# Kernel optimization log

Measured on AMD Instinct MI355X. Metric: run time of the kernel, lower is better.

The kernel has to match this reference:

```python
import jax, jax.numpy as jnp
import numpy as np

# dims
N, Lx, Ff = 2048, 168, 64          # batch, encoder seq len, encoder features
HID = 256                           # GRU hidden size
Ly, Ft, FOUT, BINS = 72, 22, 10, 8  # decoder steps, future feats, output size, rain classes
DEC_IN = Ft + FOUT                  # 32, GRUCell input = cat(y_t, p)
REG_H, CLS_H = 128, 128             # head hidden widths
BETA = 1.1                          # SmeLU beta


def smelu(x):
    # SmeLU: 0 for x<=-b, x for x>=b, (x+b)^2/(4b) in between
    return jnp.where(x >= BETA, x,
                     jnp.where(x <= -BETA, jnp.zeros_like(x),
                               (x + BETA) ** 2 / (4.0 * BETA)))


def gru_step(h, u, Wih, Whh, bih, bhh):
    # torch GRU/GRUCell gate math; Wih: (3H, in), Whh: (3H, H)
    gi = u @ Wih.T + bih
    gh = h @ Whh.T + bhh
    i_r, i_z, i_n = jnp.split(gi, 3, axis=-1)
    h_r, h_z, h_n = jnp.split(gh, 3, axis=-1)
    r = jax.nn.sigmoid(i_r + h_r)
    z = jax.nn.sigmoid(i_z + h_z)
    n = jnp.tanh(i_n + r * h_n)
    return (1.0 - z) * n + z * h


def setup_inputs() -> dict:
    key = jax.random.key(0)
    ks = jax.random.split(key, 24)
    s = 1.0 / np.sqrt(HID)

    def rn(k, shape, scale):
        return jax.random.normal(k, shape, dtype=jnp.float32) * scale

    return {
        'x_f': rn(ks[0], (N, Lx, Ff), 1.0),
        'x': rn(ks[1], (N, Lx, FOUT), 1.0),      # unused by forward (matches torch)
        'y_t': rn(ks[2], (N, Ly + 1, Ft), 1.0),
        'p': rn(ks[3], (N, Ly + 1, FOUT), 1.0),
        # encoder GRU (1 layer, unidirectional)
        'enc_Wih': rn(ks[4], (3 * HID, Ff), s), 'enc_Whh': rn(ks[5], (3 * HID, HID), s),
        'enc_bih': rn(ks[6], (3 * HID,), s), 'enc_bhh': rn(ks[7], (3 * HID,), s),
        # decoder GRUCell
        'dec_Wih': rn(ks[8], (3 * HID, DEC_IN), s), 'dec_Whh': rn(ks[9], (3 * HID, HID), s),
        'dec_bih': rn(ks[10], (3 * HID,), s), 'dec_bhh': rn(ks[11], (3 * HID,), s),
        # temphr head: HID -> REG_H -> (FOUT - BINS)
        'th_W0': rn(ks[12], (REG_H, HID), s), 'th_b0': rn(ks[13], (REG_H,), s),
        'th_W1': rn(ks[14], (FOUT - BINS, REG_H), 1.0 / np.sqrt(REG_H)), 'th_b1': rn(ks[15], (FOUT - BINS,), 0.05),
        # class head: HID -> CLS_H -> BINS
        'cl_W0': rn(ks[16], (CLS_H, HID), s), 'cl_b0': rn(ks[17], (CLS_H,), s),
        'cl_W1': rn(ks[18], (BINS, CLS_H), 1.0 / np.sqrt(CLS_H)), 'cl_b1': rn(ks[19], (BINS,), 0.05),
    }


def reference(x_f, x, y_t, p,
              enc_Wih, enc_Whh, enc_bih, enc_bhh,
              dec_Wih, dec_Whh, dec_bih, dec_bhh,
              th_W0, th_b0, th_W1, th_b1,
              cl_W0, cl_b0, cl_W1, cl_b1):
    # ---- encoder: run GRU over Lx, keep final hidden (N, HID) ----
    h0 = jnp.zeros((x_f.shape[0], HID), dtype=x_f.dtype)
    enc_xs = jnp.swapaxes(x_f, 0, 1)  # (Lx, N, Ff)

    def enc_body(h, u):
        return gru_step(h, u, enc_Wih, enc_Whh, enc_bih, enc_bhh), None

    h_enc, _ = jax.lax.scan(enc_body, h0, enc_xs)

    # ---- decoder inputs: torch loop uses cat(y_t,p) at index 0, then i-1 ----
    ytp = jnp.concatenate([y_t[:, :-1, :], p[:, :-1, :]], axis=-1)  # (N, Ly, DEC_IN)
    idx = jnp.concatenate([jnp.zeros((1,), jnp.int32), jnp.arange(Ly - 1, dtype=jnp.int32)])
    dec_in = jnp.swapaxes(ytp[:, idx, :], 0, 1)  # (Ly, N, DEC_IN)

    def dec_body(h, u):
        h2 = gru_step(h, u, dec_Wih, dec_Whh, dec_bih, dec_bhh)
        th = smelu(h2 @ th_W0.T + th_b0) @ th_W1.T + th_b1   # (N, 2)
        cl = smelu(h2 @ cl_W0.T + cl_b0) @ cl_W1.T + cl_b1   # (N, BINS)
        return h2, jnp.concatenate([th, cl], axis=-1)

    _, outs = jax.lax.scan(dec_body, h_enc, dec_in)  # (Ly, N, FOUT)
    return jnp.swapaxes(outs, 0, 1)  # (N, Ly, FOUT)
```

## Files before the change

kernel.cpp:

```cpp
#include <hip/hip_runtime.h>

typedef __bf16 v8bf __attribute__((ext_vector_type(8)));
typedef float v4f __attribute__((ext_vector_type(4)));
typedef float v4ff __attribute__((ext_vector_type(4)));
typedef unsigned short u16;
typedef unsigned int u32;

#define DEVI __device__ __forceinline__

constexpr int LX = 168, FF = 64;
constexpr int LY = 72, FT = 22, FOUTC = 10;
constexpr int HID = 256;
constexpr int HSTR = 264;
constexpr int UST2 = 40;
constexpr int SSTR = 264;

constexpr int W_EWIH = 0;
constexpr int W_EWHH = 49152;
constexpr int W_DWIH = 245760;
constexpr int W_DWHH = 270336;
constexpr int W_THW0 = 466944;
constexpr int W_THW1 = 499712;
constexpr int W_CLW0 = 499968;
constexpr int W_CLW1 = 532736;
constexpr int W_TOTAL = 533760;

DEVI u16 f2bf(float f) {
  u32 x; __builtin_memcpy(&x, &f, 4);
  return (u16)((x + 0x7FFFu + ((x >> 16) & 1u)) >> 16);
}
DEVI float sigm(float x) { return __builtin_amdgcn_rcpf(1.f + __expf(-x)); }
DEVI float tanh_(float x) {
  float e = __expf(-2.f * fabsf(x));
  return copysignf((1.f - e) * __builtin_amdgcn_rcpf(1.f + e), x);
}
DEVI float smelu_(float x) {
  if (x >= 1.1f) return x;
  if (x <= -1.1f) return 0.f;
  float u = x + 1.1f;
  return u * u * (1.f / 4.4f);
}
DEVI v8bf ld8(const u16* p) { return *reinterpret_cast<const v8bf*>(p); }
DEVI v4f ldw(const u16* p) { return *reinterpret_cast<const v4f*>(p); }
DEVI v8bf asbf(v4f x) { return __builtin_bit_cast(v8bf, x); }
DEVI void pin(v4f& x) { asm("" : "+v"(x)); }
DEVI v4f mfma16(v8bf a, v8bf b, v4f c) {
  return __builtin_amdgcn_mfma_f32_16x16x32_bf16(a, b, c, 0, 0, 0);
}
DEVI v8bf cvt2f(v4ff lo, v4ff hi) {
  v8bf r;
#pragma unroll
  for (int j = 0; j < 4; ++j) { r[j] = (__bf16)lo[j]; r[4 + j] = (__bf16)hi[j]; }
  return r;
}

__global__ void cvt_weights(const float* __restrict__ eWih, const float* __restrict__ eWhh,
                            const float* __restrict__ dWih, const float* __restrict__ dWhh,
                            const float* __restrict__ thW0, const float* __restrict__ thW1,
                            const float* __restrict__ clW0, const float* __restrict__ clW1,
                            u16* __restrict__ ws) {
  const int i = blockIdx.x * 256 + threadIdx.x;
  if (i >= W_TOTAL) return;
  const float* src; int off;
  if      (i < W_EWHH) { src = eWih; off = W_EWIH; }
  else if (i < W_DWIH) { src = eWhh; off = W_EWHH; }
  else if (i < W_DWHH) { src = dWih; off = W_DWIH; }
  else if (i < W_THW0) { src = dWhh; off = W_DWHH; }
  else if (i < W_THW1) { src = thW0; off = W_THW0; }
  else if (i < W_CLW0) { src = thW1; off = W_THW1; }
  else if (i < W_CLW1) { src = clW0; off = W_CLW0; }
  else                 { src = clW1; off = W_CLW1; }
  ws[i] = f2bf(src[i - off]);
}

__global__ __launch_bounds__(512, 2) void encdec_kernel(
    const float* __restrict__ xf, const float* __restrict__ yt, const float* __restrict__ pp,
    const float* __restrict__ ebih, const float* __restrict__ ebhh,
    const float* __restrict__ dbih, const float* __restrict__ dbhh,
    const float* __restrict__ thb0, const float* __restrict__ thb1,
    const float* __restrict__ clb0, const float* __restrict__ clb1,
    const u16* __restrict__ ws, float* __restrict__ outp) {
  __shared__ __align__(16) u16 slab[256 * SSTR];
  __shared__ __align__(16) u16 hls[2][16 * HSTR];
  __shared__ __align__(16) u16 a1x[16 * HSTR];
  __shared__ __align__(16) u16 uls[2][16 * UST2];

  const u16* eWih = ws + W_EWIH;
  const u16* eWhh = ws + W_EWHH;
  const u16* dWih = ws + W_DWIH;
  const u16* dWhh = ws + W_DWHH;
  const u16* thW0 = ws + W_THW0;
  const u16* thW1 = ws + W_THW1;
  const u16* clW0 = ws + W_CLW0;
  const u16* clW1 = ws + W_CLW1;

  const int tid = threadIdx.x;
  const int wave = tid >> 6;
  const int lane = tid & 63;
  const int col16 = lane & 15;
  const int quad = lane >> 4;
  const int n0 = blockIdx.x * 16;

  for (int i = tid; i < 16 * HSTR; i += 512) hls[0][i] = 0;

  float hreg[2][4];
#pragma unroll
  for (int j = 0; j < 2; ++j)
#pragma unroll
    for (int r = 0; r < 4; ++r) hreg[j][r] = 0.f;

  v4f wz[2][8], wn[2][8];
  float bsr[2], bsz[2], bin_[2], bhn[2];

  {
    for (int i = tid; i < 256 * 32; i += 512) {
      const int row = i >> 5, kb = (i & 31) << 3;
      *reinterpret_cast<v8bf*>(&slab[row * SSTR + kb]) = ld8(eWhh + row * HID + kb);
    }
#pragma unroll
    for (int j = 0; j < 2; ++j) {
      const int c = wave + 8 * j;
      const int mr = c * 16 + col16, mz = 256 + mr, mn = 512 + mr;
#pragma unroll
      for (int k = 0; k < 8; ++k) {
        wz[j][k] = ldw(eWhh + (size_t)mz * HID + k * 32 + quad * 8); pin(wz[j][k]);
        wn[j][k] = ldw(eWhh + (size_t)mn * HID + k * 32 + quad * 8); pin(wn[j][k]);
      }
      bsr[j] = ebih[mr] + ebhh[mr];
      bsz[j] = ebih[mz] + ebhh[mz];
      bin_[j] = ebih[mn];
      bhn[j] = ebhh[mn];
    }
    const float* xbase = xf + (size_t)(n0 + col16) * LX * FF + quad * 8;
    const u16* sp0 = slab + (wave * 16 + col16) * SSTR + quad * 8;
    const u16* sp1 = slab + ((wave + 8) * 16 + col16) * SSTR + quad * 8;

    v8bf xa0, xa1;
    {
      const v4ff x0 = *(const v4ff*)(xbase);
      const v4ff x1 = *(const v4ff*)(xbase + 4);
      const v4ff x2 = *(const v4ff*)(xbase + 32);
      const v4ff x3 = *(const v4ff*)(xbase + 36);
      xa0 = cvt2f(x0, x1);
      xa1 = cvt2f(x2, x3);
    }
    __syncthreads();

#pragma unroll 1
    for (int t = 0; t < LX; ++t) {
      const u16* hb = hls[t & 1] + col16 * HSTR + quad * 8;

      v4f az[2], ar[2], an[2], ai[2];
#pragma unroll
      for (int j = 0; j < 2; ++j) {
        az[j] = (v4f){bsz[j], bsz[j], bsz[j], bsz[j]};
        ar[j] = (v4f){bsr[j], bsr[j], bsr[j], bsr[j]};
        an[j] = (v4f){bhn[j], bhn[j], bhn[j], bhn[j]};
        ai[j] = (v4f){bin_[j], bin_[j], bin_[j], bin_[j]};
      }

      __builtin_amdgcn_s_setprio(1);
      v8bf ak = ld8(hb), ak1 = ld8(hb + 32);
#pragma unroll
      for (int k = 0; k < 8; ++k) {
        az[0] = mfma16(ak, asbf(wz[0][k]), az[0]);
        az[1] = mfma16(ak, asbf(wz[1][k]), az[1]);
        ar[0] = mfma16(ak, ld8(sp0 + k * 32), ar[0]);
        ar[1] = mfma16(ak, ld8(sp1 + k * 32), ar[1]);
        an[0] = mfma16(ak, asbf(wn[0][k]), an[0]);
        an[1] = mfma16(ak, asbf(wn[1][k]), an[1]);
        ak = ak1;
        if (k < 6) ak1 = ld8(hb + (k + 2) * 32);
      }

      const int tn = (t + 1 < LX) ? t + 1 : 0;
      const float* xr = xbase + (size_t)tn * FF;
      const v4ff x0 = *(const v4ff*)(xr);
      const v4ff x1 = *(const v4ff*)(xr + 4);
      const v4ff x2 = *(const v4ff*)(xr + 32);
      const v4ff x3 = *(const v4ff*)(xr + 36);

#pragma unroll
      for (int j = 0; j < 2; ++j) {
        const int m = (wave + 8 * j) * 16 + col16;
        const u16* pwr = eWih + (size_t)m * FF + quad * 8;
        const u16* pwz = eWih + (size_t)(256 + m) * FF + quad * 8;
        const u16* pwn = eWih + (size_t)(512 + m) * FF + quad * 8;
        az[j] = mfma16(xa0, ld8(pwz), az[j]);
        az[j] = mfma16(xa1, ld8(pwz + 32), az[j]);
        ar[j] = mfma16(xa0, ld8(pwr), ar[j]);
        ar[j] = mfma16(xa1, ld8(pwr + 32), ar[j]);
        ai[j] = mfma16(xa0, ld8(pwn), ai[j]);
        ai[j] = mfma16(xa1, ld8(pwn + 32), ai[j]);
      }
      __builtin_amdgcn_s_setprio(0);

#pragma unroll
      for (int j = 0; j < 2; ++j) {
        const int cidx = (wave + 8 * j) * 16 + col16;
#pragma unroll
        for (int r = 0; r < 4; ++r) {
          const float zg = sigm(az[j][r]);
          const float rg = sigm(ar[j][r]);
          const float ng = tanh_(ai[j][r] + rg * an[j][r]);
          hreg[j][r] = (1.f - zg) * ng + zg * hreg[j][r];
          hls[(t + 1) & 1][(quad * 4 + r) * HSTR + cidx] = f2bf(hreg[j][r]);
        }
      }
      xa0 = cvt2f(x0, x1);
      xa1 = cvt2f(x2, x3);
      __syncthreads();
    }
  }

  {
    for (int i = tid; i < 256 * 32; i += 512) {
      const int row = i >> 5, kb = (i & 31) << 3;
      *reinterpret_cast<v8bf*>(&slab[row * SSTR + kb]) = ld8(dWhh + row * HID + kb);
    }
    float hb0[2];
#pragma unroll
    for (int j = 0; j < 2; ++j) {
      const int c = wave + 8 * j;
      const int mr = c * 16 + col16, mz = 256 + mr, mn = 512 + mr;
#pragma unroll
      for (int k = 0; k < 8; ++k) {
        wz[j][k] = ldw(dWhh + (size_t)mz * HID + k * 32 + quad * 8); pin(wz[j][k]);
        wn[j][k] = ldw(dWhh + (size_t)mn * HID + k * 32 + quad * 8); pin(wn[j][k]);
      }
      bsr[j] = dbih[mr] + dbhh[mr];
      bsz[j] = dbih[mz] + dbhh[mz];
      bin_[j] = dbih[mn];
      bhn[j] = dbhh[mn];
      const int ml = wave * 16 + col16;
      hb0[j] = (j == 0) ? thb0[ml] : clb0[ml];
    }
    const bool w1th = (col16 < 2);
    const bool w1cl = (col16 >= 2 && col16 < FOUTC);
    const float b1v = w1th ? thb1[col16] : (w1cl ? clb1[col16 - 2] : 0.f);
    const u16* sp0 = slab + (wave * 16 + col16) * SSTR + quad * 8;
    const u16* sp1 = slab + ((wave + 8) * 16 + col16) * SSTR + quad * 8;

    const int srr = tid >> 5, scc = tid & 31;
    const size_t ybase = (size_t)(n0 + srr) * (LY + 1);
    {
      const float v = (scc < FT) ? yt[ybase * FT + scc] : pp[ybase * FOUTC + (scc - FT)];
      uls[0][srr * UST2 + scc] = f2bf(v);
    }
    __syncthreads();

#pragma unroll 1
    for (int t = 0; t < LY; ++t) {
      float un = 0.f;
      if (t + 1 < LY)
        un = (scc < FT) ? yt[(ybase + t) * FT + scc]
                        : pp[(ybase + t) * FOUTC + (scc - FT)];
      const v8bf ua = ld8(uls[t & 1] + col16 * UST2 + quad * 8);
      const u16* hb = hls[0] + col16 * HSTR + quad * 8;
      v8bf a[8];
#pragma unroll
      for (int k = 0; k < 8; ++k) a[k] = ld8(hb + k * 32);
      __syncthreads();

      if (wave == 0 && t >= 2) {
        const u16* arow = ((t & 1) ? a1x : hls[1]) + col16 * HSTR + quad * 8;
        v4f acc = {b1v, b1v, b1v, b1v};
#pragma unroll
        for (int kt = 0; kt < 8; ++kt) {
          v8bf b;
#pragma unroll
          for (int j = 0; j < 8; ++j) b[j] = (__bf16)0.0f;
          if (kt < 4) { if (w1th) b = ld8(thW1 + col16 * 128 + kt * 32 + quad * 8); }
          else        { if (w1cl) b = ld8(clW1 + (col16 - 2) * 128 + (kt - 4) * 32 + quad * 8); }
          acc = mfma16(ld8(arow + kt * 32), b, acc);
        }
        if (col16 < FOUTC) {
#pragma unroll
          for (int r = 0; r < 4; ++r)
            outp[((size_t)(n0 + quad * 4 + r) * LY + (t - 2)) * FOUTC + col16] = acc[r];
        }
      }

      v4f az[2], ar[2], an[2], ai[2];
#pragma unroll
      for (int j = 0; j < 2; ++j) {
        az[j] = (v4f){bsz[j], bsz[j], bsz[j], bsz[j]};
        ar[j] = (v4f){bsr[j], bsr[j], bsr[j], bsr[j]};
        an[j] = (v4f){bhn[j], bhn[j], bhn[j], bhn[j]};
        ai[j] = (v4f){bin_[j], bin_[j], bin_[j], bin_[j]};
      }
      __builtin_amdgcn_s_setprio(1);
#pragma unroll
      for (int k = 0; k < 8; ++k) {
        az[0] = mfma16(a[k], asbf(wz[0][k]), az[0]);
        az[1] = mfma16(a[k], asbf(wz[1][k]), az[1]);
        ar[0] = mfma16(a[k], ld8(sp0 + k * 32), ar[0]);
        ar[1] = mfma16(a[k], ld8(sp1 + k * 32), ar[1]);
        an[0] = mfma16(a[k], asbf(wn[0][k]), an[0]);
        an[1] = mfma16(a[k], asbf(wn[1][k]), an[1]);
      }
#pragma unroll
      for (int j = 0; j < 2; ++j) {
        const int m = (wave + 8 * j) * 16 + col16;
        az[j] = mfma16(ua, ld8(dWih + (size_t)(256 + m) * 32 + quad * 8), az[j]);
        ar[j] = mfma16(ua, ld8(dWih + (size_t)m * 32 + quad * 8), ar[j]);
        ai[j] = mfma16(ua, ld8(dWih + (size_t)(512 + m) * 32 + quad * 8), ai[j]);
      }
      __builtin_amdgcn_s_setprio(0);
#pragma unroll
      for (int j = 0; j < 2; ++j) {
        const int cidx = (wave + 8 * j) * 16 + col16;
#pragma unroll
        for (int r = 0; r < 4; ++r) {
          const float zg = sigm(az[j][r]);
          const float rg = sigm(ar[j][r]);
          const float ng = tanh_(ai[j][r] + rg * an[j][r]);
          hreg[j][r] = (1.f - zg) * ng + zg * hreg[j][r];
          hls[0][(quad * 4 + r) * HSTR + cidx] = f2bf(hreg[j][r]);
        }
      }

      if (t >= 1) {
        u16* a1w = ((t - 1) & 1) ? a1x : hls[1];
#pragma unroll
        for (int j = 0; j < 2; ++j) {
          const u16* W0 = (j == 0) ? thW0 : clW0;
          const u16* pw = W0 + (size_t)(wave * 16 + col16) * HID + quad * 8;
          v4f acc = {hb0[j], hb0[j], hb0[j], hb0[j]};
#pragma unroll
          for (int k = 0; k < 8; ++k) acc = mfma16(a[k], ld8(pw + k * 32), acc);
          const int c = wave + 8 * j;
#pragma unroll
          for (int r = 0; r < 4; ++r)
            a1w[(quad * 4 + r) * HSTR + c * 16 + col16] = f2bf(smelu_(acc[r]));
        }
      }
      if (t + 1 < LY) uls[(t + 1) & 1][srr * UST2 + scc] = f2bf(un);
      __syncthreads();
    }

    {
      const u16* h2b = hls[0] + col16 * HSTR + quad * 8;
      v8bf ah2[8];
#pragma unroll
      for (int k = 0; k < 8; ++k) ah2[k] = ld8(h2b + k * 32);
      u16* a1w = ((LY - 1) & 1) ? a1x : hls[1];
#pragma unroll
      for (int j = 0; j < 2; ++j) {
        const u16* W0 = (j == 0) ? thW0 : clW0;
        const u16* pw = W0 + (size_t)(wave * 16 + col16) * HID + quad * 8;
        v4f acc = {hb0[j], hb0[j], hb0[j], hb0[j]};
#pragma unroll
        for (int k = 0; k < 8; ++k) acc = mfma16(ah2[k], ld8(pw + k * 32), acc);
        const int c = wave + 8 * j;
#pragma unroll
        for (int r = 0; r < 4; ++r)
          a1w[(quad * 4 + r) * HSTR + c * 16 + col16] = f2bf(smelu_(acc[r]));
      }
      if (wave == 0) {
        const u16* arow = (((LY - 2) & 1) ? a1x : hls[1]) + col16 * HSTR + quad * 8;
        v4f acc = {b1v, b1v, b1v, b1v};
#pragma unroll
        for (int kt = 0; kt < 8; ++kt) {
          v8bf b;
#pragma unroll
          for (int j = 0; j < 8; ++j) b[j] = (__bf16)0.0f;
          if (kt < 4) { if (w1th) b = ld8(thW1 + col16 * 128 + kt * 32 + quad * 8); }
          else        { if (w1cl) b = ld8(clW1 + (col16 - 2) * 128 + (kt - 4) * 32 + quad * 8); }
          acc = mfma16(ld8(arow + kt * 32), b, acc);
        }
        if (col16 < FOUTC) {
#pragma unroll
          for (int r = 0; r < 4; ++r)
            outp[((size_t)(n0 + quad * 4 + r) * LY + (LY - 2)) * FOUTC + col16] = acc[r];
        }
      }
      __syncthreads();
      if (wave == 0) {
        const u16* arow = (((LY - 1) & 1) ? a1x : hls[1]) + col16 * HSTR + quad * 8;
        v4f acc = {b1v, b1v, b1v, b1v};
#pragma unroll
        for (int kt = 0; kt < 8; ++kt) {
          v8bf b;
#pragma unroll
          for (int j = 0; j < 8; ++j) b[j] = (__bf16)0.0f;
          if (kt < 4) { if (w1th) b = ld8(thW1 + col16 * 128 + kt * 32 + quad * 8); }
          else        { if (w1cl) b = ld8(clW1 + (col16 - 2) * 128 + (kt - 4) * 32 + quad * 8); }
          acc = mfma16(ld8(arow + kt * 32), b, acc);
        }
        if (col16 < FOUTC) {
#pragma unroll
          for (int r = 0; r < 4; ++r)
            outp[((size_t)(n0 + quad * 4 + r) * LY + (LY - 1)) * FOUTC + col16] = acc[r];
        }
      }
    }
  }
}

extern "C" void kernel_launch(void* const* d_in, const int* in_sizes, int n_in,
                              void* d_out, int out_size, void* d_ws, size_t ws_size,
                              hipStream_t stream) {
  (void)in_sizes; (void)n_in; (void)ws_size; (void)out_size;
  const float* xf   = (const float*)d_in[0];
  const float* yt   = (const float*)d_in[2];
  const float* pp   = (const float*)d_in[3];
  const float* eWih = (const float*)d_in[4];
  const float* eWhh = (const float*)d_in[5];
  const float* ebih = (const float*)d_in[6];
  const float* ebhh = (const float*)d_in[7];
  const float* dWih = (const float*)d_in[8];
  const float* dWhh = (const float*)d_in[9];
  const float* dbih = (const float*)d_in[10];
  const float* dbhh = (const float*)d_in[11];
  const float* thW0 = (const float*)d_in[12];
  const float* thb0 = (const float*)d_in[13];
  const float* thW1 = (const float*)d_in[14];
  const float* thb1 = (const float*)d_in[15];
  const float* clW0 = (const float*)d_in[16];
  const float* clb0 = (const float*)d_in[17];
  const float* clW1 = (const float*)d_in[18];
  const float* clb1 = (const float*)d_in[19];
  float* outp = (float*)d_out;
  u16* ws = (u16*)d_ws;

  cvt_weights<<<dim3((W_TOTAL + 255) / 256), dim3(256), 0, stream>>>(
      eWih, eWhh, dWih, dWhh, thW0, thW1, clW0, clW1, ws);
  encdec_kernel<<<dim3(128), dim3(512), 0, stream>>>(
      xf, yt, pp, ebih, ebhh, dbih, dbhh, thb0, thb1, clb0, clb1, ws, outp);
}
```

Before: 1.344 ms.

## Halve workgroup to 4 waves, keep more Whh rows in registers

After: 1.970 ms. 1.47x slower.

```diff
diff --git a/kernel.cpp b/kernel.cpp
--- a/kernel.cpp
+++ b/kernel.cpp
@@ -73,16 +73,16 @@
   ws[i] = f2bf(src[i - off]);
 }
 
-__global__ __launch_bounds__(512, 2) void encdec_kernel(
+__global__ __launch_bounds__(256, 1) void encdec_kernel(
     const float* __restrict__ xf, const float* __restrict__ yt, const float* __restrict__ pp,
     const float* __restrict__ ebih, const float* __restrict__ ebhh,
     const float* __restrict__ dbih, const float* __restrict__ dbhh,
     const float* __restrict__ thb0, const float* __restrict__ thb1,
     const float* __restrict__ clb0, const float* __restrict__ clb1,
     const u16* __restrict__ ws, float* __restrict__ outp) {
-  __shared__ __align__(16) u16 slab[256 * SSTR];
+  __shared__ __align__(16) u16 slab[128 * SSTR];
   __shared__ __align__(16) u16 hls[2][16 * HSTR];
-  __shared__ __align__(16) u16 a1x[16 * HSTR];
+  __shared__ __align__(16) u16 a1d[2][16 * HSTR];
   __shared__ __align__(16) u16 uls[2][16 * UST2];
 
   const u16* eWih = ws + W_EWIH;
@@ -101,25 +101,30 @@
   const int quad = lane >> 4;
   const int n0 = blockIdx.x * 16;
 
-  for (int i = tid; i < 16 * HSTR; i += 512) hls[0][i] = 0;
-
-  float hreg[2][4];
-#pragma unroll
-  for (int j = 0; j < 2; ++j)
+  float hreg[4][4];
+#pragma unroll
+  for (int j = 0; j < 4; ++j)
 #pragma unroll
     for (int r = 0; r < 4; ++r) hreg[j][r] = 0.f;
 
-  v4f wz[2][8], wn[2][8];
-  float bsr[2], bsz[2], bin_[2], bhn[2];
+  v4f wz[4][8], wn[4][8], wr[2][8];
+  float bsr[4], bsz[4], bin_[4], bhn[4];
+
+  const u16* sp2 = slab + ((wave * 2 + 0) * 16 + col16) * SSTR + quad * 8;
+  const u16* sp3 = slab + ((wave * 2 + 1) * 16 + col16) * SSTR + quad * 8;
 
   {
-    for (int i = tid; i < 256 * 32; i += 512) {
-      const int row = i >> 5, kb = (i & 31) << 3;
-      *reinterpret_cast<v8bf*>(&slab[row * SSTR + kb]) = ld8(eWhh + row * HID + kb);
-    }
-#pragma unroll
-    for (int j = 0; j < 2; ++j) {
-      const int c = wave + 8 * j;
+    for (int i = tid; i < 128 * 32; i += 256) {
+      const int sr = i >> 5, kb = (i & 31) << 3;
+      const int ct = sr >> 4;
+      const int c = (ct >> 1) * 4 + 2 + (ct & 1);
+      const int m = c * 16 + (sr & 15);
+      *reinterpret_cast<v8bf*>(&slab[sr * SSTR + kb]) = ld8(eWhh + (size_t)m * HID + kb);
+    }
+    for (int i = tid; i < 16 * HSTR; i += 256) hls[0][i] = 0;
+#pragma unroll
+    for (int j = 0; j < 4; ++j) {
+      const int c = wave * 4 + j;
       const int mr = c * 16 + col16, mz = 256 + mr, mn = 512 + mr;
 #pragma unroll
       for (int k = 0; k < 8; ++k) {
@@ -131,9 +136,15 @@
       bin_[j] = ebih[mn];
       bhn[j] = ebhh[mn];
     }
+#pragma unroll
+    for (int j = 0; j < 2; ++j) {
+      const int mr = (wave * 4 + j) * 16 + col16;
+#pragma unroll
+      for (int k = 0; k < 8; ++k) {
+        wr[j][k] = ldw(eWhh + (size_t)mr * HID + k * 32 + quad * 8); pin(wr[j][k]);
+      }
+    }
     const float* xbase = xf + (size_t)(n0 + col16) * LX * FF + quad * 8;
-    const u16* sp0 = slab + (wave * 16 + col16) * SSTR + quad * 8;
-    const u16* sp1 = slab + ((wave + 8) * 16 + col16) * SSTR + quad * 8;
 
     v8bf xa0, xa1;
     {
@@ -149,43 +160,40 @@
 #pragma unroll 1
     for (int t = 0; t < LX; ++t) {
       const u16* hb = hls[t & 1] + col16 * HSTR + quad * 8;
-
-      v4f az[2], ar[2], an[2], ai[2];
-#pragma unroll
-      for (int j = 0; j < 2; ++j) {
+      v8bf a[8];
+#pragma unroll
+      for (int k = 0; k < 8; ++k) a[k] = ld8(hb + k * 32);
+
+      v4f az[4], ar[4], an[4];
+#pragma unroll
+      for (int j = 0; j < 4; ++j) {
         az[j] = (v4f){bsz[j], bsz[j], bsz[j], bsz[j]};
         ar[j] = (v4f){bsr[j], bsr[j], bsr[j], bsr[j]};
         an[j] = (v4f){bhn[j], bhn[j], bhn[j], bhn[j]};
-        ai[j] = (v4f){bin_[j], bin_[j], bin_[j], bin_[j]};
-      }
-
-      __builtin_amdgcn_s_setprio(1);
-      v8bf ak = ld8(hb), ak1 = ld8(hb + 32);
-#pragma unroll
-      for (int k = 0; k < 8; ++k) {
-        az[0] = mfma16(ak, asbf(wz[0][k]), az[0]);
-        az[1] = mfma16(ak, asbf(wz[1][k]), az[1]);
-        ar[0] = mfma16(ak, ld8(sp0 + k * 32), ar[0]);
-        ar[1] = mfma16(ak, ld8(sp1 + k * 32), ar[1]);
-        an[0] = mfma16(ak, asbf(wn[0][k]), an[0]);
-        an[1] = mfma16(ak, asbf(wn[1][k]), an[1]);
-        ak = ak1;
-        if (k < 6) ak1 = ld8(hb + (k + 2) * 32);
-      }
-
-      const int tn = (t + 1 < LX) ? t + 1 : 0;
-      const float* xr = xbase + (size_t)tn * FF;
-      const v4ff x0 = *(const v4ff*)(xr);
-      const v4ff x1 = *(const v4ff*)(xr + 4);
-      const v4ff x2 = *(const v4ff*)(xr + 32);
-      const v4ff x3 = *(const v4ff*)(xr + 36);
-
-#pragma unroll
-      for (int j = 0; j < 2; ++j) {
-        const int m = (wave + 8 * j) * 16 + col16;
+      }
+#pragma unroll
+      for (int k = 0; k < 8; ++k) {
+        az[0] = mfma16(a[k], asbf(wz[0][k]), az[0]);
+        az[1] = mfma16(a[k], asbf(wz[1][k]), az[1]);
+        az[2] = mfma16(a[k], asbf(wz[2][k]), az[2]);
+        az[3] = mfma16(a[k], asbf(wz[3][k]), az[3]);
+        ar[0] = mfma16(a[k], asbf(wr[0][k]), ar[0]);
+        ar[1] = mfma16(a[k], asbf(wr[1][k]), ar[1]);
+        ar[2] = mfma16(a[k], ld8(sp2 + k * 32), ar[2]);
+        ar[3] = mfma16(a[k], ld8(sp3 + k * 32), ar[3]);
+        an[0] = mfma16(a[k], asbf(wn[0][k]), an[0]);
+        an[1] = mfma16(a[k], asbf(wn[1][k]), an[1]);
+        an[2] = mfma16(a[k], asbf(wn[2][k]), an[2]);
+        an[3] = mfma16(a[k], asbf(wn[3][k]), an[3]);
+      }
+      v4f ai[4];
+#pragma unroll
+      for (int j = 0; j < 4; ++j) {
+        const int m = (wave * 4 + j) * 16 + col16;
         const u16* pwr = eWih + (size_t)m * FF + quad * 8;
         const u16* pwz = eWih + (size_t)(256 + m) * FF + quad * 8;
         const u16* pwn = eWih + (size_t)(512 + m) * FF + quad * 8;
+        ai[j] = (v4f){bin_[j], bin_[j], bin_[j], bin_[j]};
         az[j] = mfma16(xa0, ld8(pwz), az[j]);
         az[j] = mfma16(xa1, ld8(pwz + 32), az[j]);
         ar[j] = mfma16(xa0, ld8(pwr), ar[j]);
@@ -193,18 +201,23 @@
         ai[j] = mfma16(xa0, ld8(pwn), ai[j]);
         ai[j] = mfma16(xa1, ld8(pwn + 32), ai[j]);
       }
-      __builtin_amdgcn_s_setprio(0);
-
-#pragma unroll
-      for (int j = 0; j < 2; ++j) {
-        const int cidx = (wave + 8 * j) * 16 + col16;
+      const int tn = (t + 1 < LX) ? t + 1 : t;
+      const float* xr = xbase + (size_t)tn * FF;
+      const v4ff x0 = *(const v4ff*)(xr);
+      const v4ff x1 = *(const v4ff*)(xr + 4);
+      const v4ff x2 = *(const v4ff*)(xr + 32);
+      const v4ff x3 = *(const v4ff*)(xr + 36);
+
+#pragma unroll
+      for (int j = 0; j < 4; ++j) {
+        const int cx = (wave * 4 + j) * 16 + col16;
 #pragma unroll
         for (int r = 0; r < 4; ++r) {
           const float zg = sigm(az[j][r]);
           const float rg = sigm(ar[j][r]);
           const float ng = tanh_(ai[j][r] + rg * an[j][r]);
           hreg[j][r] = (1.f - zg) * ng + zg * hreg[j][r];
-          hls[(t + 1) & 1][(quad * 4 + r) * HSTR + cidx] = f2bf(hreg[j][r]);
+          hls[(t + 1) & 1][(quad * 4 + r) * HSTR + cx] = f2bf(hreg[j][r]);
         }
       }
       xa0 = cvt2f(x0, x1);
@@ -214,14 +227,16 @@
   }
 
   {
-    for (int i = tid; i < 256 * 32; i += 512) {
-      const int row = i >> 5, kb = (i & 31) << 3;
-      *reinterpret_cast<v8bf*>(&slab[row * SSTR + kb]) = ld8(dWhh + row * HID + kb);
-    }
-    float hb0[2];
-#pragma unroll
-    for (int j = 0; j < 2; ++j) {
-      const int c = wave + 8 * j;
+    for (int i = tid; i < 128 * 32; i += 256) {
+      const int sr = i >> 5, kb = (i & 31) << 3;
+      const int ct = sr >> 4;
+      const int c = (ct >> 1) * 4 + 2 + (ct & 1);
+      const int m = c * 16 + (sr & 15);
+      *reinterpret_cast<v8bf*>(&slab[sr * SSTR + kb]) = ld8(dWhh + (size_t)m * HID + kb);
+    }
+#pragma unroll
+    for (int j = 0; j < 4; ++j) {
+      const int c = wave * 4 + j;
       const int mr = c * 16 + col16, mz = 256 + mr, mn = 512 + mr;
 #pragma unroll
       for (int k = 0; k < 8; ++k) {
@@ -232,169 +247,154 @@
       bsz[j] = dbih[mz] + dbhh[mz];
       bin_[j] = dbih[mn];
       bhn[j] = dbhh[mn];
-      const int ml = wave * 16 + col16;
-      hb0[j] = (j == 0) ? thb0[ml] : clb0[ml];
+    }
+#pragma unroll
+    for (int j = 0; j < 2; ++j) {
+      const int mr = (wave * 4 + j) * 16 + col16;
+#pragma unroll
+      for (int k = 0; k < 8; ++k) {
+        wr[j][k] = ldw(dWhh + (size_t)mr * HID + k * 32 + quad * 8); pin(wr[j][k]);
+      }
+    }
+    const u16* pW0[4]; float hb0[4];
+#pragma unroll
+    for (int j = 0; j < 4; ++j) {
+      const int h = wave * 4 + j;
+      const int row = (h & 7) * 16 + col16;
+      pW0[j] = ((h < 8) ? thW0 : clW0) + (size_t)row * HID + quad * 8;
+      hb0[j] = (h < 8) ? thb0[row] : clb0[row];
     }
     const bool w1th = (col16 < 2);
     const bool w1cl = (col16 >= 2 && col16 < FOUTC);
     const float b1v = w1th ? thb1[col16] : (w1cl ? clb1[col16 - 2] : 0.f);
-    const u16* sp0 = slab + (wave * 16 + col16) * SSTR + quad * 8;
-    const u16* sp1 = slab + ((wave + 8) * 16 + col16) * SSTR + quad * 8;
-
-    const int srr = tid >> 5, scc = tid & 31;
-    const size_t ybase = (size_t)(n0 + srr) * (LY + 1);
+
+    const int scc = tid & 31;
+    const int srr = tid >> 5;
     {
-      const float v = (scc < FT) ? yt[ybase * FT + scc] : pp[ybase * FOUTC + (scc - FT)];
-      uls[0][srr * UST2 + scc] = f2bf(v);
-    }
+#pragma unroll
+      for (int rr = srr; rr < 16; rr += 8) {
+        const size_t yb = (size_t)(n0 + rr) * (LY + 1);
+        const float v = (scc < FT) ? yt[yb * FT + scc] : pp[yb * FOUTC + (scc - FT)];
+        uls[0][rr * UST2 + scc] = f2bf(v);
+      }
+    }
+
+    auto gemm2 = [&](int s) {
+      const u16* arow = a1d[s & 1] + col16 * HSTR + quad * 8;
+      v4f acc = {b1v, b1v, b1v, b1v};
+#pragma unroll
+      for (int kt = 0; kt < 8; ++kt) {
+        v8bf b;
+#pragma unroll
+        for (int j = 0; j < 8; ++j) b[j] = (__bf16)0.0f;
+        if (kt < 4) { if (w1th) b = ld8(thW1 + col16 * 128 + kt * 32 + quad * 8); }
+        else        { if (w1cl) b = ld8(clW1 + (col16 - 2) * 128 + (kt - 4) * 32 + quad * 8); }
+        acc = mfma16(ld8(arow + kt * 32), b, acc);
+      }
+      if (col16 < FOUTC) {
+#pragma unroll
+        for (int r = 0; r < 4; ++r)
+          outp[((size_t)(n0 + quad * 4 + r) * LY + s) * FOUTC + col16] = acc[r];
+      }
+    };
+
+    auto gemm1 = [&](const u16* hbase, u16* a1w) {
+      const u16* hA = hbase + col16 * HSTR + quad * 8;
+      v4f acc[4];
+#pragma unroll
+      for (int j = 0; j < 4; ++j) acc[j] = (v4f){hb0[j], hb0[j], hb0[j], hb0[j]};
+#pragma unroll
+      for (int k = 0; k < 8; ++k) {
+        const v8bf hk = ld8(hA + k * 32);
+        acc[0] = mfma16(hk, ld8(pW0[0] + k * 32), acc[0]);
+        acc[1] = mfma16(hk, ld8(pW0[1] + k * 32), acc[1]);
+        acc[2] = mfma16(hk, ld8(pW0[2] + k * 32), acc[2]);
+        acc[3] = mfma16(hk, ld8(pW0[3] + k * 32), acc[3]);
+      }
+#pragma unroll
+      for (int j = 0; j < 4; ++j) {
+        const int hcol = (wave * 4 + j) * 16 + col16;
+#pragma unroll
+        for (int r = 0; r < 4; ++r)
+          a1w[(quad * 4 + r) * HSTR + hcol] = f2bf(smelu_(acc[j][r]));
+      }
+    };
+
     __syncthreads();
 
 #pragma unroll 1
     for (int t = 0; t < LY; ++t) {
-      float un = 0.f;
-      if (t + 1 < LY)
-        un = (scc < FT) ? yt[(ybase + t) * FT + scc]
-                        : pp[(ybase + t) * FOUTC + (scc - FT)];
+      float un0 = 0.f, un1 = 0.f;
+      if (t + 1 < LY) {
+        const size_t yb0 = (size_t)(n0 + srr) * (LY + 1) + t;
+        const size_t yb1 = (size_t)(n0 + srr + 8) * (LY + 1) + t;
+        un0 = (scc < FT) ? yt[yb0 * FT + scc] : pp[yb0 * FOUTC + (scc - FT)];
+        un1 = (scc < FT) ? yt[yb1 * FT + scc] : pp[yb1 * FOUTC + (scc - FT)];
+      }
+
+      if (wave == (t & 3) && t >= 2) gemm2(t - 2);
+
       const v8bf ua = ld8(uls[t & 1] + col16 * UST2 + quad * 8);
-      const u16* hb = hls[0] + col16 * HSTR + quad * 8;
-      v8bf a[8];
-#pragma unroll
-      for (int k = 0; k < 8; ++k) a[k] = ld8(hb + k * 32);
-      __syncthreads();
-
-      if (wave == 0 && t >= 2) {
-        const u16* arow = ((t & 1) ? a1x : hls[1]) + col16 * HSTR + quad * 8;
-        v4f acc = {b1v, b1v, b1v, b1v};
-#pragma unroll
-        for (int kt = 0; kt < 8; ++kt) {
-          v8bf b;
-#pragma unroll
-          for (int j = 0; j < 8; ++j) b[j] = (__bf16)0.0f;
-          if (kt < 4) { if (w1th) b = ld8(thW1 + col16 * 128 + kt * 32 + quad * 8); }
-          else        { if (w1cl) b = ld8(clW1 + (col16 - 2) * 128 + (kt - 4) * 32 + quad * 8); }
-          acc = mfma16(ld8(arow + kt * 32), b, acc);
-        }
-        if (col16 < FOUTC) {
-#pragma unroll
-          for (int r = 0; r < 4; ++r)
-            outp[((size_t)(n0 + quad * 4 + r) * LY + (t - 2)) * FOUTC + col16] = acc[r];
-        }
-      }
-
-      v4f az[2], ar[2], an[2], ai[2];
-#pragma unroll
-      for (int j = 0; j < 2; ++j) {
+      const u16* hb = hls[t & 1] + col16 * HSTR + quad * 8;
+
+      v4f az[4], ar[4], an[4];
+#pragma unroll
+      for (int j = 0; j < 4; ++j) {
         az[j] = (v4f){bsz[j], bsz[j], bsz[j], bsz[j]};
         ar[j] = (v4f){bsr[j], bsr[j], bsr[j], bsr[j]};
         an[j] = (v4f){bhn[j], bhn[j], bhn[j], bhn[j]};
+      }
+#pragma unroll
+      for (int k = 0; k < 8; ++k) {
+        const v8bf ak = ld8(hb + k * 32);
+        az[0] = mfma16(ak, asbf(wz[0][k]), az[0]);
+        az[1] = mfma16(ak, asbf(wz[1][k]), az[1]);
+        az[2] = mfma16(ak, asbf(wz[2][k]), az[2]);
+        az[3] = mfma16(ak, asbf(wz[3][k]), az[3]);
+        ar[0] = mfma16(ak, asbf(wr[0][k]), ar[0]);
+        ar[1] = mfma16(ak, asbf(wr[1][k]), ar[1]);
+        ar[2] = mfma16(ak, ld8(sp2 + k * 32), ar[2]);
+        ar[3] = mfma16(ak, ld8(sp3 + k * 32), ar[3]);
+        an[0] = mfma16(ak, asbf(wn[0][k]), an[0]);
+        an[1] = mfma16(ak, asbf(wn[1][k]), an[1]);
+        an[2] = mfma16(ak, asbf(wn[2][k]), an[2]);
+        an[3] = mfma16(ak, asbf(wn[3][k]), an[3]);
+      }
+      v4f ai[4];
+#pragma unroll
+      for (int j = 0; j < 4; ++j) {
+        const int m = (wave * 4 + j) * 16 + col16;
         ai[j] = (v4f){bin_[j], bin_[j], bin_[j], bin_[j]};
-      }
-      __builtin_amdgcn_s_setprio(1);
-#pragma unroll
-      for (int k = 0; k < 8; ++k) {
-        az[0] = mfma16(a[k], asbf(wz[0][k]), az[0]);
-        az[1] = mfma16(a[k], asbf(wz[1][k]), az[1]);
-        ar[0] = mfma16(a[k], ld8(sp0 + k * 32), ar[0]);
-        ar[1] = mfma16(a[k], ld8(sp1 + k * 32), ar[1]);
-        an[0] = mfma16(a[k], asbf(wn[0][k]), an[0]);
-        an[1] = mfma16(a[k], asbf(wn[1][k]), an[1]);
-      }
-#pragma unroll
-      for (int j = 0; j < 2; ++j) {
-        const int m = (wave + 8 * j) * 16 + col16;
         az[j] = mfma16(ua, ld8(dWih + (size_t)(256 + m) * 32 + quad * 8), az[j]);
         ar[j] = mfma16(ua, ld8(dWih + (size_t)m * 32 + quad * 8), ar[j]);
         ai[j] = mfma16(ua, ld8(dWih + (size_t)(512 + m) * 32 + quad * 8), ai[j]);
       }
-      __builtin_amdgcn_s_setprio(0);
-#pragma unroll
-      for (int j = 0; j < 2; ++j) {
-        const int cidx = (wave + 8 * j) * 16 + col16;
+#pragma unroll
+      for (int j = 0; j < 4; ++j) {
+        const int cx = (wave * 4 + j) * 16 + col16;
 #pragma unroll
         for (int r = 0; r < 4; ++r) {
           const float zg = sigm(az[j][r]);
           const float rg = sigm(ar[j][r]);
           const float ng = tanh_(ai[j][r] + rg * an[j][r]);
           hreg[j][r] = (1.f - zg) * ng + zg * hreg[j][r];
-          hls[0][(quad * 4 + r) * HSTR + cidx] = f2bf(hreg[j][r]);
+          hls[(t + 1) & 1][(quad * 4 + r) * HSTR + cx] = f2bf(hreg[j][r]);
         }
       }
 
-      if (t >= 1) {
-        u16* a1w = ((t - 1) & 1) ? a1x : hls[1];
-#pragma unroll
-        for (int j = 0; j < 2; ++j) {
-          const u16* W0 = (j == 0) ? thW0 : clW0;
-          const u16* pw = W0 + (size_t)(wave * 16 + col16) * HID + quad * 8;
-          v4f acc = {hb0[j], hb0[j], hb0[j], hb0[j]};
-#pragma unroll
-          for (int k = 0; k < 8; ++k) acc = mfma16(a[k], ld8(pw + k * 32), acc);
-          const int c = wave + 8 * j;
-#pragma unroll
-          for (int r = 0; r < 4; ++r)
-            a1w[(quad * 4 + r) * HSTR + c * 16 + col16] = f2bf(smelu_(acc[r]));
-        }
-      }
-      if (t + 1 < LY) uls[(t + 1) & 1][srr * UST2 + scc] = f2bf(un);
+      if (t >= 1) gemm1(hls[t & 1], a1d[(t - 1) & 1]);
+
+      if (t + 1 < LY) {
+        uls[(t + 1) & 1][srr * UST2 + scc] = f2bf(un0);
+        uls[(t + 1) & 1][(srr + 8) * UST2 + scc] = f2bf(un1);
+      }
       __syncthreads();
     }
 
-    {
-      const u16* h2b = hls[0] + col16 * HSTR + quad * 8;
-      v8bf ah2[8];
-#pragma unroll
-      for (int k = 0; k < 8; ++k) ah2[k] = ld8(h2b + k * 32);
-      u16* a1w = ((LY - 1) & 1) ? a1x : hls[1];
-#pragma unroll
-      for (int j = 0; j < 2; ++j) {
-        const u16* W0 = (j == 0) ? thW0 : clW0;
-        const u16* pw = W0 + (size_t)(wave * 16 + col16) * HID + quad * 8;
-        v4f acc = {hb0[j], hb0[j], hb0[j], hb0[j]};
-#pragma unroll
-        for (int k = 0; k < 8; ++k) acc = mfma16(ah2[k], ld8(pw + k * 32), acc);
-        const int c = wave + 8 * j;
-#pragma unroll
-        for (int r = 0; r < 4; ++r)
-          a1w[(quad * 4 + r) * HSTR + c * 16 + col16] = f2bf(smelu_(acc[r]));
-      }
-      if (wave == 0) {
-        const u16* arow = (((LY - 2) & 1) ? a1x : hls[1]) + col16 * HSTR + quad * 8;
-        v4f acc = {b1v, b1v, b1v, b1v};
-#pragma unroll
-        for (int kt = 0; kt < 8; ++kt) {
-          v8bf b;
-#pragma unroll
-          for (int j = 0; j < 8; ++j) b[j] = (__bf16)0.0f;
-          if (kt < 4) { if (w1th) b = ld8(thW1 + col16 * 128 + kt * 32 + quad * 8); }
-          else        { if (w1cl) b = ld8(clW1 + (col16 - 2) * 128 + (kt - 4) * 32 + quad * 8); }
-          acc = mfma16(ld8(arow + kt * 32), b, acc);
-        }
-        if (col16 < FOUTC) {
-#pragma unroll
-          for (int r = 0; r < 4; ++r)
-            outp[((size_t)(n0 + quad * 4 + r) * LY + (LY - 2)) * FOUTC + col16] = acc[r];
-        }
-      }
-      __syncthreads();
-      if (wave == 0) {
-        const u16* arow = (((LY - 1) & 1) ? a1x : hls[1]) + col16 * HSTR + quad * 8;
-        v4f acc = {b1v, b1v, b1v, b1v};
-#pragma unroll
-        for (int kt = 0; kt < 8; ++kt) {
-          v8bf b;
-#pragma unroll
-          for (int j = 0; j < 8; ++j) b[j] = (__bf16)0.0f;
-          if (kt < 4) { if (w1th) b = ld8(thW1 + col16 * 128 + kt * 32 + quad * 8); }
-          else        { if (w1cl) b = ld8(clW1 + (col16 - 2) * 128 + (kt - 4) * 32 + quad * 8); }
-          acc = mfma16(ld8(arow + kt * 32), b, acc);
-        }
-        if (col16 < FOUTC) {
-#pragma unroll
-          for (int r = 0; r < 4; ++r)
-            outp[((size_t)(n0 + quad * 4 + r) * LY + (LY - 1)) * FOUTC + col16] = acc[r];
-        }
-      }
-    }
+    gemm1(hls[LY & 1], a1d[(LY - 1) & 1]);
+    if (wave == 0) gemm2(LY - 2);
+    __syncthreads();
+    if (wave == 0) gemm2(LY - 1);
   }
 }
 
@@ -426,6 +426,6 @@
 
   cvt_weights<<<dim3((W_TOTAL + 255) / 256), dim3(256), 0, stream>>>(
       eWih, eWhh, dWih, dWhh, thW0, thW1, clW0, clW1, ws);
-  encdec_kernel<<<dim3(128), dim3(512), 0, stream>>>(
+  encdec_kernel<<<dim3(128), dim3(256), 0, stream>>>(
       xf, yt, pp, ebih, ebhh, dbih, dbhh, thb0, thb1, clb0, clb1, ws, outp);
 }
```

## Drop LDS weight slab, stream r-gate weights from global, pre-pad head weights

Applied to the files above, without the earlier changes.

New measurement: 2.247 ms. 67.2% more time.

```diff
diff --git a/kernel.cpp b/kernel.cpp
--- a/kernel.cpp
+++ b/kernel.cpp
@@ -13,7 +13,6 @@
 constexpr int HID = 256;
 constexpr int HSTR = 264;
 constexpr int UST2 = 40;
-constexpr int SSTR = 264;
 
 constexpr int W_EWIH = 0;
 constexpr int W_EWHH = 49152;
@@ -23,7 +22,8 @@
 constexpr int W_THW1 = 499712;
 constexpr int W_CLW0 = 499968;
 constexpr int W_CLW1 = 532736;
-constexpr int W_TOTAL = 533760;
+constexpr int W_W1F  = 533760;
+constexpr int W_TOTALF = 537856;
 
 DEVI u16 f2bf(float f) {
   u32 x; __builtin_memcpy(&x, &f, 4);
@@ -60,7 +60,15 @@
                             const float* __restrict__ clW0, const float* __restrict__ clW1,
                             u16* __restrict__ ws) {
   const int i = blockIdx.x * 256 + threadIdx.x;
-  if (i >= W_TOTAL) return;
+  if (i >= W_TOTALF) return;
+  if (i >= W_W1F) {
+    const int r = i - W_W1F, c = r >> 8, k = r & 255;
+    float v = 0.f;
+    if (c < 2 && k < 128) v = thW1[c * 128 + k];
+    else if (c >= 2 && c < FOUTC && k >= 128) v = clW1[(c - 2) * 128 + (k - 128)];
+    ws[i] = f2bf(v);
+    return;
+  }
   const float* src; int off;
   if      (i < W_EWHH) { src = eWih; off = W_EWIH; }
   else if (i < W_DWIH) { src = eWhh; off = W_EWHH; }
@@ -80,7 +88,6 @@
     const float* __restrict__ thb0, const float* __restrict__ thb1,
     const float* __restrict__ clb0, const float* __restrict__ clb1,
     const u16* __restrict__ ws, float* __restrict__ outp) {
-  __shared__ __align__(16) u16 slab[256 * SSTR];
   __shared__ __align__(16) u16 hls[2][16 * HSTR];
   __shared__ __align__(16) u16 a1x[16 * HSTR];
   __shared__ __align__(16) u16 uls[2][16 * UST2];
@@ -90,9 +97,8 @@
   const u16* dWih = ws + W_DWIH;
   const u16* dWhh = ws + W_DWHH;
   const u16* thW0 = ws + W_THW0;
-  const u16* thW1 = ws + W_THW1;
   const u16* clW0 = ws + W_CLW0;
-  const u16* clW1 = ws + W_CLW1;
+  const u16* w1f  = ws + W_W1F;
 
   const int tid = threadIdx.x;
   const int wave = tid >> 6;
@@ -112,15 +118,14 @@
   v4f wz[2][8], wn[2][8];
   float bsr[2], bsz[2], bin_[2], bhn[2];
 
+  const int mr0 = wave * 16 + col16;
+  const int mr1 = (wave + 8) * 16 + col16;
+
   {
-    for (int i = tid; i < 256 * 32; i += 512) {
-      const int row = i >> 5, kb = (i & 31) << 3;
-      *reinterpret_cast<v8bf*>(&slab[row * SSTR + kb]) = ld8(eWhh + row * HID + kb);
-    }
 #pragma unroll
     for (int j = 0; j < 2; ++j) {
-      const int c = wave + 8 * j;
-      const int mr = c * 16 + col16, mz = 256 + mr, mn = 512 + mr;
+      const int mr = (j == 0) ? mr0 : mr1;
+      const int mz = 256 + mr, mn = 512 + mr;
 #pragma unroll
       for (int k = 0; k < 8; ++k) {
         wz[j][k] = ldw(eWhh + (size_t)mz * HID + k * 32 + quad * 8); pin(wz[j][k]);
@@ -132,60 +137,49 @@
       bhn[j] = ebhh[mn];
     }
     const float* xbase = xf + (size_t)(n0 + col16) * LX * FF + quad * 8;
-    const u16* sp0 = slab + (wave * 16 + col16) * SSTR + quad * 8;
-    const u16* sp1 = slab + ((wave + 8) * 16 + col16) * SSTR + quad * 8;
-
-    v8bf xa0, xa1;
-    {
-      const v4ff x0 = *(const v4ff*)(xbase);
-      const v4ff x1 = *(const v4ff*)(xbase + 4);
-      const v4ff x2 = *(const v4ff*)(xbase + 32);
-      const v4ff x3 = *(const v4ff*)(xbase + 36);
-      xa0 = cvt2f(x0, x1);
-      xa1 = cvt2f(x2, x3);
-    }
+    const u16* wr0p = eWhh + (size_t)mr0 * HID + quad * 8;
+    const u16* wr1p = eWhh + (size_t)mr1 * HID + quad * 8;
     __syncthreads();
 
 #pragma unroll 1
     for (int t = 0; t < LX; ++t) {
-      const u16* hb = hls[t & 1] + col16 * HSTR + quad * 8;
-
-      v4f az[2], ar[2], an[2], ai[2];
-#pragma unroll
-      for (int j = 0; j < 2; ++j) {
-        az[j] = (v4f){bsz[j], bsz[j], bsz[j], bsz[j]};
-        ar[j] = (v4f){bsr[j], bsr[j], bsr[j], bsr[j]};
-        an[j] = (v4f){bhn[j], bhn[j], bhn[j], bhn[j]};
-        ai[j] = (v4f){bin_[j], bin_[j], bin_[j], bin_[j]};
-      }
-
-      __builtin_amdgcn_s_setprio(1);
-      v8bf ak = ld8(hb), ak1 = ld8(hb + 32);
-#pragma unroll
-      for (int k = 0; k < 8; ++k) {
-        az[0] = mfma16(ak, asbf(wz[0][k]), az[0]);
-        az[1] = mfma16(ak, asbf(wz[1][k]), az[1]);
-        ar[0] = mfma16(ak, ld8(sp0 + k * 32), ar[0]);
-        ar[1] = mfma16(ak, ld8(sp1 + k * 32), ar[1]);
-        an[0] = mfma16(ak, asbf(wn[0][k]), an[0]);
-        an[1] = mfma16(ak, asbf(wn[1][k]), an[1]);
-        ak = ak1;
-        if (k < 6) ak1 = ld8(hb + (k + 2) * 32);
-      }
-
-      const int tn = (t + 1 < LX) ? t + 1 : 0;
-      const float* xr = xbase + (size_t)tn * FF;
+      const float* xr = xbase + (size_t)t * FF;
       const v4ff x0 = *(const v4ff*)(xr);
       const v4ff x1 = *(const v4ff*)(xr + 4);
       const v4ff x2 = *(const v4ff*)(xr + 32);
       const v4ff x3 = *(const v4ff*)(xr + 36);
-
+      const u16* hb = hls[t & 1] + col16 * HSTR + quad * 8;
+      v8bf a[8];
+#pragma unroll
+      for (int k = 0; k < 8; ++k) a[k] = ld8(hb + k * 32);
+
+      v4f az[2], ar[2], an[2];
+#pragma unroll
+      for (int j = 0; j < 2; ++j) {
+        az[j] = (v4f){bsz[j], bsz[j], bsz[j], bsz[j]};
+        ar[j] = (v4f){bsr[j], bsr[j], bsr[j], bsr[j]};
+        an[j] = (v4f){bhn[j], bhn[j], bhn[j], bhn[j]};
+      }
+#pragma unroll
+      for (int k = 0; k < 8; ++k) {
+        if (k == 4) __builtin_amdgcn_sched_barrier(0);
+        az[0] = mfma16(a[k], asbf(wz[0][k]), az[0]);
+        az[1] = mfma16(a[k], asbf(wz[1][k]), az[1]);
+        ar[0] = mfma16(a[k], ld8(wr0p + k * 32), ar[0]);
+        ar[1] = mfma16(a[k], ld8(wr1p + k * 32), ar[1]);
+        an[0] = mfma16(a[k], asbf(wn[0][k]), an[0]);
+        an[1] = mfma16(a[k], asbf(wn[1][k]), an[1]);
+      }
+      const v8bf xa0 = cvt2f(x0, x1);
+      const v8bf xa1 = cvt2f(x2, x3);
+      v4f ai[2];
 #pragma unroll
       for (int j = 0; j < 2; ++j) {
         const int m = (wave + 8 * j) * 16 + col16;
         const u16* pwr = eWih + (size_t)m * FF + quad * 8;
         const u16* pwz = eWih + (size_t)(256 + m) * FF + quad * 8;
         const u16* pwn = eWih + (size_t)(512 + m) * FF + quad * 8;
+        ai[j] = (v4f){bin_[j], bin_[j], bin_[j], bin_[j]};
         az[j] = mfma16(xa0, ld8(pwz), az[j]);
         az[j] = mfma16(xa1, ld8(pwz + 32), az[j]);
         ar[j] = mfma16(xa0, ld8(pwr), ar[j]);
@@ -193,8 +187,6 @@
         ai[j] = mfma16(xa0, ld8(pwn), ai[j]);
         ai[j] = mfma16(xa1, ld8(pwn + 32), ai[j]);
       }
-      __builtin_amdgcn_s_setprio(0);
-
 #pragma unroll
       for (int j = 0; j < 2; ++j) {
         const int cidx = (wave + 8 * j) * 16 + col16;
@@ -207,22 +199,16 @@
           hls[(t + 1) & 1][(quad * 4 + r) * HSTR + cidx] = f2bf(hreg[j][r]);
         }
       }
-      xa0 = cvt2f(x0, x1);
-      xa1 = cvt2f(x2, x3);
       __syncthreads();
     }
   }
 
   {
-    for (int i = tid; i < 256 * 32; i += 512) {
-      const int row = i >> 5, kb = (i & 31) << 3;
-      *reinterpret_cast<v8bf*>(&slab[row * SSTR + kb]) = ld8(dWhh + row * HID + kb);
-    }
     float hb0[2];
 #pragma unroll
     for (int j = 0; j < 2; ++j) {
-      const int c = wave + 8 * j;
-      const int mr = c * 16 + col16, mz = 256 + mr, mn = 512 + mr;
+      const int mr = (j == 0) ? mr0 : mr1;
+      const int mz = 256 + mr, mn = 512 + mr;
 #pragma unroll
       for (int k = 0; k < 8; ++k) {
         wz[j][k] = ldw(dWhh + (size_t)mz * HID + k * 32 + quad * 8); pin(wz[j][k]);
@@ -235,11 +221,11 @@
       const int ml = wave * 16 + col16;
       hb0[j] = (j == 0) ? thb0[ml] : clb0[ml];
     }
-    const bool w1th = (col16 < 2);
-    const bool w1cl = (col16 >= 2 && col16 < FOUTC);
-    const float b1v = w1th ? thb1[col16] : (w1cl ? clb1[col16 - 2] : 0.f);
-    const u16* sp0 = slab + (wave * 16 + col16) * SSTR + quad * 8;
-    const u16* sp1 = slab + ((wave + 8) * 16 + col16) * SSTR + quad * 8;
+    const float b1v = (col16 < 2) ? thb1[col16]
+                    : (col16 < FOUTC) ? clb1[col16 - 2] : 0.f;
+    const u16* w1p = w1f + col16 * HID + quad * 8;
+    const u16* wr0p = dWhh + (size_t)mr0 * HID + quad * 8;
+    const u16* wr1p = dWhh + (size_t)mr1 * HID + quad * 8;
 
     const int srr = tid >> 5, scc = tid & 31;
     const size_t ybase = (size_t)(n0 + srr) * (LY + 1);
@@ -247,6 +233,19 @@
       const float v = (scc < FT) ? yt[ybase * FT + scc] : pp[ybase * FOUTC + (scc - FT)];
       uls[0][srr * UST2 + scc] = f2bf(v);
     }
+
+    auto gemm2 = [&](int s, const u16* a1b) {
+      const u16* arow = a1b + col16 * HSTR + quad * 8;
+      v4f acc = {b1v, b1v, b1v, b1v};
+#pragma unroll
+      for (int kt = 0; kt < 8; ++kt)
+        acc = mfma16(ld8(arow + kt * 32), ld8(w1p + kt * 32), acc);
+      if (col16 < FOUTC) {
+#pragma unroll
+        for (int r = 0; r < 4; ++r)
+          outp[((size_t)(n0 + quad * 4 + r) * LY + s) * FOUTC + col16] = acc[r];
+      }
+    };
     __syncthreads();
 
 #pragma unroll 1
@@ -262,51 +261,34 @@
       for (int k = 0; k < 8; ++k) a[k] = ld8(hb + k * 32);
       __syncthreads();
 
-      if (wave == 0 && t >= 2) {
-        const u16* arow = ((t & 1) ? a1x : hls[1]) + col16 * HSTR + quad * 8;
-        v4f acc = {b1v, b1v, b1v, b1v};
-#pragma unroll
-        for (int kt = 0; kt < 8; ++kt) {
-          v8bf b;
-#pragma unroll
-          for (int j = 0; j < 8; ++j) b[j] = (__bf16)0.0f;
-          if (kt < 4) { if (w1th) b = ld8(thW1 + col16 * 128 + kt * 32 + quad * 8); }
-          else        { if (w1cl) b = ld8(clW1 + (col16 - 2) * 128 + (kt - 4) * 32 + quad * 8); }
-          acc = mfma16(ld8(arow + kt * 32), b, acc);
-        }
-        if (col16 < FOUTC) {
-#pragma unroll
-          for (int r = 0; r < 4; ++r)
-            outp[((size_t)(n0 + quad * 4 + r) * LY + (t - 2)) * FOUTC + col16] = acc[r];
-        }
-      }
-
-      v4f az[2], ar[2], an[2], ai[2];
+      if (wave == 0 && t >= 2) gemm2(t - 2, (t & 1) ? a1x : hls[1]);
+
+      v4f az[2], ar[2], an[2];
 #pragma unroll
       for (int j = 0; j < 2; ++j) {
         az[j] = (v4f){bsz[j], bsz[j], bsz[j], bsz[j]};
         ar[j] = (v4f){bsr[j], bsr[j], bsr[j], bsr[j]};
         an[j] = (v4f){bhn[j], bhn[j], bhn[j], bhn[j]};
-        ai[j] = (v4f){bin_[j], bin_[j], bin_[j], bin_[j]};
-      }
-      __builtin_amdgcn_s_setprio(1);
+      }
 #pragma unroll
       for (int k = 0; k < 8; ++k) {
+        if (k == 4) __builtin_amdgcn_sched_barrier(0);
         az[0] = mfma16(a[k], asbf(wz[0][k]), az[0]);
         az[1] = mfma16(a[k], asbf(wz[1][k]), az[1]);
-        ar[0] = mfma16(a[k], ld8(sp0 + k * 32), ar[0]);
-        ar[1] = mfma16(a[k], ld8(sp1 + k * 32), ar[1]);
+        ar[0] = mfma16(a[k], ld8(wr0p + k * 32), ar[0]);
+        ar[1] = mfma16(a[k], ld8(wr1p + k * 32), ar[1]);
         an[0] = mfma16(a[k], asbf(wn[0][k]), an[0]);
         an[1] = mfma16(a[k], asbf(wn[1][k]), an[1]);
       }
+      v4f ai[2];
 #pragma unroll
       for (int j = 0; j < 2; ++j) {
         const int m = (wave + 8 * j) * 16 + col16;
+        ai[j] = (v4f){bin_[j], bin_[j], bin_[j], bin_[j]};
         az[j] = mfma16(ua, ld8(dWih + (size_t)(256 + m) * 32 + quad * 8), az[j]);
         ar[j] = mfma16(ua, ld8(dWih + (size_t)m * 32 + quad * 8), ar[j]);
         ai[j] = mfma16(ua, ld8(dWih + (size_t)(512 + m) * 32 + quad * 8), ai[j]);
       }
-      __builtin_amdgcn_s_setprio(0);
 #pragma unroll
       for (int j = 0; j < 2; ++j) {
         const int cidx = (wave + 8 * j) * 16 + col16;
@@ -357,43 +339,9 @@
         for (int r = 0; r < 4; ++r)
           a1w[(quad * 4 + r) * HSTR + c * 16 + col16] = f2bf(smelu_(acc[r]));
       }
-      if (wave == 0) {
-        const u16* arow = (((LY - 2) & 1) ? a1x : hls[1]) + col16 * HSTR + quad * 8;
-        v4f acc = {b1v, b1v, b1v, b1v};
-#pragma unroll
-        for (int kt = 0; kt < 8; ++kt) {
-          v8bf b;
-#pragma unroll
-          for (int j = 0; j < 8; ++j) b[j] = (__bf16)0.0f;
-          if (kt < 4) { if (w1th) b = ld8(thW1 + col16 * 128 + kt * 32 + quad * 8); }
-          else        { if (w1cl) b = ld8(clW1 + (col16 - 2) * 128 + (kt - 4) * 32 + quad * 8); }
-          acc = mfma16(ld8(arow + kt * 32), b, acc);
-        }
-        if (col16 < FOUTC) {
-#pragma unroll
-          for (int r = 0; r < 4; ++r)
-            outp[((size_t)(n0 + quad * 4 + r) * LY + (LY - 2)) * FOUTC + col16] = acc[r];
-        }
-      }
+      if (wave == 0) gemm2(LY - 2, ((LY - 2) & 1) ? a1x : hls[1]);
       __syncthreads();
-      if (wave == 0) {
-        const u16* arow = (((LY - 1) & 1) ? a1x : hls[1]) + col16 * HSTR + quad * 8;
-        v4f acc = {b1v, b1v, b1v, b1v};
-#pragma unroll
-        for (int kt = 0; kt < 8; ++kt) {
-          v8bf b;
-#pragma unroll
-          for (int j = 0; j < 8; ++j) b[j] = (__bf16)0.0f;
-          if (kt < 4) { if (w1th) b = ld8(thW1 + col16 * 128 + kt * 32 + quad * 8); }
-          else        { if (w1cl) b = ld8(clW1 + (col16 - 2) * 128 + (kt - 4) * 32 + quad * 8); }
-          acc = mfma16(ld8(arow + kt * 32), b, acc);
-        }
-        if (col16 < FOUTC) {
-#pragma unroll
-          for (int r = 0; r < 4; ++r)
-            outp[((size_t)(n0 + quad * 4 + r) * LY + (LY - 1)) * FOUTC + col16] = acc[r];
-        }
-      }
+      if (wave == 0) gemm2(LY - 1, ((LY - 1) & 1) ? a1x : hls[1]);
     }
   }
 }
@@ -424,7 +372,7 @@
   float* outp = (float*)d_out;
   u16* ws = (u16*)d_ws;
 
-  cvt_weights<<<dim3((W_TOTAL + 255) / 256), dim3(256), 0, stream>>>(
+  cvt_weights<<<dim3((W_TOTALF + 255) / 256), dim3(256), 0, stream>>>(
       eWih, eWhh, dWih, dWhh, thW0, thW1, clW0, clW1, ws);
   encdec_kernel<<<dim3(128), dim3(512), 0, stream>>>(
       xf, yt, pp, ebih, ebhh, dbih, dbhh, thb0, thb1, clb0, clb1, ws, outp);
```
